# Optimization experiments

Measured on AMD Instinct MI355X. Metric: run time of the kernel, lower is better.

The kernel has to match this reference:

```python
import jax, jax.numpy as jnp
import numpy as np

NUM_HEADS = 10
DICT = 20  # attention_dictionary_size
BATCH = 262144


def setup_inputs() -> dict:
    key = jax.random.key(0)
    ks = jax.random.split(key, 6)
    x = jax.random.normal(ks[0], (BATCH, DICT), dtype=jnp.float32)
    # torch nn.Linear(20, 200, bias=False) weights: shape [out, in] = [200, 20]
    W1 = jax.random.normal(ks[1], (NUM_HEADS * DICT, DICT), dtype=jnp.float32) * 0.1
    W2 = jax.random.normal(ks[2], (NUM_HEADS * DICT, DICT), dtype=jnp.float32) * 0.1
    W3 = jax.random.normal(ks[3], (NUM_HEADS * DICT, DICT), dtype=jnp.float32) * 0.1
    W4 = jax.random.normal(ks[4], (NUM_HEADS * DICT, DICT), dtype=jnp.float32) * 0.1
    gamma = jax.random.normal(ks[5], (1,), dtype=jnp.float32)
    return {"x": x, "W1": W1, "W2": W2, "W3": W3, "W4": W4, "gamma": gamma}


def reference(x, W1, W2, W3, W4, gamma):
    B = x.shape[0]
    m = 1
    inp = x[:, None, :]                                   # [B, 1, 20]
    # Four bias-free projections: y = x @ W.T -> [B, 1, 200]
    q = (inp @ W1.T).reshape(NUM_HEADS, B, m, DICT)       # faithful .view (mixes batch/head)
    k = (inp @ W2.T).reshape(NUM_HEADS, B, DICT, m)
    v = (inp @ W3.T).reshape(NUM_HEADS, B, m, DICT)
    inner = q @ k                                         # [10, B, 1, 1]
    att = jax.nn.softmax(inner, axis=-1)                  # length-1 softmax -> ones (faithful)
    res = jnp.swapaxes(att, -1, -2) @ v                   # [10, B, 1, 20]
    res = res.reshape(B, m, NUM_HEADS * DICT)             # [B, 1, 200]
    out = jax.nn.relu(gamma * res + inp @ W4.T)           # [B, 1, 200]
    return out
```

## Files before the change

### kernel.cpp

```cpp
#include <hip/hip_runtime.h>


#define BATCH          262144
#define DICT           20
#define COLS           200
#define NTHREADS       256
#define ROWS_PER_BLOCK 128
#define NBLOCKS        (BATCH / ROWS_PER_BLOCK)

__global__ __launch_bounds__(NTHREADS)
void attn_collapsed_kernel(const float* __restrict__ x,
                           const float* __restrict__ W3,
                           const float* __restrict__ W4,
                           const float* __restrict__ gamma,
                           float* __restrict__ out)
{
    __shared__ float4 ldsM[COLS * 5];

    const int t = threadIdx.x;
    const float g = gamma[0];

    const float4* w3 = (const float4*)W3;
    const float4* w4 = (const float4*)W4;
    for (int i = t; i < COLS * 5; i += NTHREADS) {
        float4 a = w3[i], b = w4[i], m;
        m.x = fmaf(g, a.x, b.x);
        m.y = fmaf(g, a.y, b.y);
        m.z = fmaf(g, a.z, b.z);
        m.w = fmaf(g, a.w, b.w);
        ldsM[i] = m;
    }
    __syncthreads();

    const int row     = blockIdx.x * ROWS_PER_BLOCK + (t & 127);
    const int colbase = (t >> 7) * 100;

    float4 xv[5];
    {
        const float4* xr = (const float4*)(x + row * DICT);
#pragma unroll
        for (int i = 0; i < 5; ++i) xv[i] = xr[i];
    }

    float4* op = (float4*)(out + row * COLS + colbase);

#pragma unroll 5
    for (int c = 0; c < 25; ++c) {
        const float4* wp = &ldsM[(colbase + 4 * c) * 5];
        float4 acc;
        float* accp = (float*)&acc;
#pragma unroll
        for (int cc = 0; cc < 4; ++cc) {
            float p0 = 0.f, p1 = 0.f;
#pragma unroll
            for (int kk = 0; kk < 5; ++kk) {
                float4 w = wp[cc * 5 + kk];
                p0 = fmaf(w.x, xv[kk].x, p0);
                p1 = fmaf(w.y, xv[kk].y, p1);
                p0 = fmaf(w.z, xv[kk].z, p0);
                p1 = fmaf(w.w, xv[kk].w, p1);
            }
            accp[cc] = fmaxf(p0 + p1, 0.f);
        }
        op[c] = acc;
    }
}

extern "C" void kernel_launch(void* const* d_in, const int* in_sizes, int n_in,
                              void* d_out, int out_size, void* d_ws, size_t ws_size,
                              hipStream_t stream) {
    const float* x     = (const float*)d_in[0];
    const float* W3    = (const float*)d_in[3];
    const float* W4    = (const float*)d_in[4];
    const float* gamma = (const float*)d_in[5];
    float* out = (float*)d_out;

    attn_collapsed_kernel<<<NBLOCKS, NTHREADS, 0, stream>>>(x, W3, W4, gamma, out);
}
```

Baseline: 290.0 us.

## Remap threads to output columns for coalesced stores and register-resident weights

Reassigns work so each thread owns one float4 of output columns and walks 32 rows, instead of one row per thread with strided column writes. Consecutive threads now write consecutive float4s of a row, so stores are coalesced. Each thread keeps its 80 weight values in registers rather than reading LDS per row, and x rows are prefetched one iteration ahead. In exchange, 56 of the 256 threads per block sit idle, x loads become broadcast reads of the same row across threads, and register pressure rises.

```diff
diff --git a/kernel.cpp b/kernel.cpp
--- a/kernel.cpp
+++ b/kernel.cpp
@@ -5,11 +5,14 @@
 #define DICT           20
 #define COLS           200
 #define NTHREADS       256
+#define NGROUPS        4
+#define ACTIVE         (50 * NGROUPS)
 #define ROWS_PER_BLOCK 128
+#define ROWS_PER_GROUP (ROWS_PER_BLOCK / NGROUPS)
 #define NBLOCKS        (BATCH / ROWS_PER_BLOCK)
 
 __global__ __launch_bounds__(NTHREADS)
-void attn_collapsed_kernel(const float* __restrict__ x,
+void attn_coalesced_kernel(const float* __restrict__ x,
                            const float* __restrict__ W3,
                            const float* __restrict__ W4,
                            const float* __restrict__ gamma,
@@ -32,37 +35,56 @@
     }
     __syncthreads();
 
-    const int row     = blockIdx.x * ROWS_PER_BLOCK + (t & 127);
-    const int colbase = (t >> 7) * 100;
+    if (t >= ACTIVE) return;
+
+    const int cf4 = t % 50;
+    const int grp = t / 50;
+
+    float4 m[4][5];
+    {
+        const float4* mp = &ldsM[cf4 * 20];
+#pragma unroll
+        for (int c = 0; c < 4; ++c)
+#pragma unroll
+            for (int k = 0; k < 5; ++k)
+                m[c][k] = mp[c * 5 + k];
+    }
+
+    const int row0 = blockIdx.x * ROWS_PER_BLOCK + grp * ROWS_PER_GROUP;
+    const float4* xr = (const float4*)(x + (size_t)row0 * DICT);
+    float4* op = (float4*)(out + (size_t)row0 * COLS) + cf4;
 
     float4 xv[5];
-    {
-        const float4* xr = (const float4*)(x + row * DICT);
 #pragma unroll
-        for (int i = 0; i < 5; ++i) xv[i] = xr[i];
-    }
+    for (int k = 0; k < 5; ++k) xv[k] = xr[k];
 
-    float4* op = (float4*)(out + row * COLS + colbase);
+    for (int r = 0; r < ROWS_PER_GROUP; ++r) {
+        float4 xn[5];
+        if (r + 1 < ROWS_PER_GROUP) {
+            const float4* xq = xr + (r + 1) * 5;
+#pragma unroll
+            for (int k = 0; k < 5; ++k) xn[k] = xq[k];
+        }
 
-#pragma unroll 5
-    for (int c = 0; c < 25; ++c) {
-        const float4* wp = &ldsM[(colbase + 4 * c) * 5];
         float4 acc;
-        float* accp = (float*)&acc;
+        float* ap = (float*)&acc;
 #pragma unroll
-        for (int cc = 0; cc < 4; ++cc) {
+        for (int c = 0; c < 4; ++c) {
             float p0 = 0.f, p1 = 0.f;
 #pragma unroll
-            for (int kk = 0; kk < 5; ++kk) {
-                float4 w = wp[cc * 5 + kk];
-                p0 = fmaf(w.x, xv[kk].x, p0);
-                p1 = fmaf(w.y, xv[kk].y, p1);
-                p0 = fmaf(w.z, xv[kk].z, p0);
-                p1 = fmaf(w.w, xv[kk].w, p1);
+            for (int k = 0; k < 5; ++k) {
+                p0 = fmaf(m[c][k].x, xv[k].x, p0);
+                p1 = fmaf(m[c][k].y, xv[k].y, p1);
+                p0 = fmaf(m[c][k].z, xv[k].z, p0);
+                p1 = fmaf(m[c][k].w, xv[k].w, p1);
             }
-            accp[cc] = fmaxf(p0 + p1, 0.f);
+            ap[c] = fmaxf(p0 + p1, 0.f);
         }
-        op[c] = acc;
+
+        op[r * 50] = acc;
+
+#pragma unroll
+        for (int k = 0; k < 5; ++k) xv[k] = xn[k];
     }
 }
 
@@ -75,5 +97,5 @@
     const float* gamma = (const float*)d_in[5];
     float* out = (float*)d_out;
 
-    attn_collapsed_kernel<<<NBLOCKS, NTHREADS, 0, stream>>>(x, W3, W4, gamma, out);
+    attn_coalesced_kernel<<<NBLOCKS, NTHREADS, 0, stream>>>(x, W3, W4, gamma, out);
 }
```

Result: slower. 334.8 us (+15.4%).

## Keep weights in registers, stage x in LDS, write contiguous columns per row

Applied to the files above, without the earlier changes.

The kernel now gives each thread two fixed output columns. Their fused gamma*W3+W4 weights are held in registers, and the block's x rows are staged in LDS. Before, each thread owned a row and wrote 100 strided columns. Now a wavefront writes contiguous float2 spans across one row, which coalesces the dominant output stores and removes the per-row weight reads from LDS. In exchange, 56 of 256 threads exit idle, each thread recomputes its weights from global memory, and the launch bounds hint changes.

```diff
diff --git a/kernel.cpp b/kernel.cpp
--- a/kernel.cpp
+++ b/kernel.cpp
@@ -5,64 +5,81 @@
 #define DICT           20
 #define COLS           200
 #define NTHREADS       256
+#define CPT            100
+#define NGROUPS        2
+#define ACTIVE         (CPT * NGROUPS)
 #define ROWS_PER_BLOCK 128
+#define ROWS_PER_GROUP (ROWS_PER_BLOCK / NGROUPS)
 #define NBLOCKS        (BATCH / ROWS_PER_BLOCK)
 
-__global__ __launch_bounds__(NTHREADS)
-void attn_collapsed_kernel(const float* __restrict__ x,
-                           const float* __restrict__ W3,
-                           const float* __restrict__ W4,
-                           const float* __restrict__ gamma,
-                           float* __restrict__ out)
+__global__ __launch_bounds__(NTHREADS, 4)
+void attn_v5_kernel(const float* __restrict__ x,
+                    const float* __restrict__ W3,
+                    const float* __restrict__ W4,
+                    const float* __restrict__ gamma,
+                    float* __restrict__ out)
 {
-    __shared__ float4 ldsM[COLS * 5];
+    __shared__ float4 ldsX[ROWS_PER_BLOCK * 5];
 
     const int t = threadIdx.x;
-    const float g = gamma[0];
 
-    const float4* w3 = (const float4*)W3;
-    const float4* w4 = (const float4*)W4;
-    for (int i = t; i < COLS * 5; i += NTHREADS) {
-        float4 a = w3[i], b = w4[i], m;
-        m.x = fmaf(g, a.x, b.x);
-        m.y = fmaf(g, a.y, b.y);
-        m.z = fmaf(g, a.z, b.z);
-        m.w = fmaf(g, a.w, b.w);
-        ldsM[i] = m;
-    }
+    const float4* xg = (const float4*)(x + (size_t)blockIdx.x * ROWS_PER_BLOCK * DICT);
+    for (int i = t; i < ROWS_PER_BLOCK * 5; i += NTHREADS)
+        ldsX[i] = xg[i];
     __syncthreads();
 
-    const int row     = blockIdx.x * ROWS_PER_BLOCK + (t & 127);
-    const int colbase = (t >> 7) * 100;
+    if (t >= ACTIVE) return;
 
-    float4 xv[5];
+    const float g   = gamma[0];
+    const int   c2  = t % CPT;
+    const int   grp = t / CPT;
+
+    float4 m0[5], m1[5];
     {
-        const float4* xr = (const float4*)(x + row * DICT);
+        const float4* a0 = (const float4*)(W3 + (2 * c2 + 0) * DICT);
+        const float4* b0 = (const float4*)(W4 + (2 * c2 + 0) * DICT);
+        const float4* a1 = (const float4*)(W3 + (2 * c2 + 1) * DICT);
+        const float4* b1 = (const float4*)(W4 + (2 * c2 + 1) * DICT);
 #pragma unroll
-        for (int i = 0; i < 5; ++i) xv[i] = xr[i];
+        for (int k = 0; k < 5; ++k) {
+            float4 p = a0[k], q = b0[k], r;
+            r.x = fmaf(g, p.x, q.x); r.y = fmaf(g, p.y, q.y);
+            r.z = fmaf(g, p.z, q.z); r.w = fmaf(g, p.w, q.w);
+            m0[k] = r;
+            float4 s = a1[k], u = b1[k], v;
+            v.x = fmaf(g, s.x, u.x); v.y = fmaf(g, s.y, u.y);
+            v.z = fmaf(g, s.z, u.z); v.w = fmaf(g, s.w, u.w);
+            m1[k] = v;
+        }
     }
 
-    float4* op = (float4*)(out + row * COLS + colbase);
+    const int row0 = blockIdx.x * ROWS_PER_BLOCK + grp * ROWS_PER_GROUP;
+    const float4* xl = &ldsX[grp * ROWS_PER_GROUP * 5];
+    float* ob = out + (size_t)row0 * COLS + 2 * c2;
 
-#pragma unroll 5
-    for (int c = 0; c < 25; ++c) {
-        const float4* wp = &ldsM[(colbase + 4 * c) * 5];
-        float4 acc;
-        float* accp = (float*)&acc;
+#pragma unroll 2
+    for (int r = 0; r < ROWS_PER_GROUP; ++r) {
+        float4 xv[5];
 #pragma unroll
-        for (int cc = 0; cc < 4; ++cc) {
-            float p0 = 0.f, p1 = 0.f;
+        for (int k = 0; k < 5; ++k) xv[k] = xl[r * 5 + k];
+
+        float p0 = 0.f, p1 = 0.f, q0 = 0.f, q1 = 0.f;
 #pragma unroll
-            for (int kk = 0; kk < 5; ++kk) {
-                float4 w = wp[cc * 5 + kk];
-                p0 = fmaf(w.x, xv[kk].x, p0);
-                p1 = fmaf(w.y, xv[kk].y, p1);
-                p0 = fmaf(w.z, xv[kk].z, p0);
-                p1 = fmaf(w.w, xv[kk].w, p1);
-            }
-            accp[cc] = fmaxf(p0 + p1, 0.f);
+        for (int k = 0; k < 5; ++k) {
+            p0 = fmaf(m0[k].x, xv[k].x, p0);
+            p1 = fmaf(m0[k].y, xv[k].y, p1);
+            p0 = fmaf(m0[k].z, xv[k].z, p0);
+            p1 = fmaf(m0[k].w, xv[k].w, p1);
+            q0 = fmaf(m1[k].x, xv[k].x, q0);
+            q1 = fmaf(m1[k].y, xv[k].y, q1);
+            q0 = fmaf(m1[k].z, xv[k].z, q0);
+            q1 = fmaf(m1[k].w, xv[k].w, q1);
         }
-        op[c] = acc;
+        float2 o;
+        o.x = fmaxf(p0 + p1, 0.f);
+        o.y = fmaxf(q0 + q1, 0.f);
+
+        *(float2*)(ob + (size_t)r * COLS) = o;
     }
 }
 
@@ -75,5 +92,5 @@
     const float* gamma = (const float*)d_in[5];
     float* out = (float*)d_out;
 
-    attn_collapsed_kernel<<<NBLOCKS, NTHREADS, 0, stream>>>(x, W3, W4, gamma, out);
+    attn_v5_kernel<<<NBLOCKS, NTHREADS, 0, stream>>>(x, W3, W4, gamma, out);
 }
```

New measurement: 253.5 us. -12.6%, faster.

## Keep combined weights in registers and write output rows coalesced per wave

Applied to the files above, without the earlier changes.

Each lane now holds four columns of the fused gamma*W3+W4 matrix in registers, and each wave walks 32 rows staged in LDS. A wave's store instruction writes one contiguous 800-byte output row, where before each thread wrote 100 strided floats. Loads and stores are marked nontemporal, and the next row's x is loaded while the current row is computed. This costs heavy register use and leaves 14 of 64 lanes idle.

```diff
diff --git a/kernel.cpp b/kernel.cpp
--- a/kernel.cpp
+++ b/kernel.cpp
@@ -6,64 +6,91 @@
 #define COLS           200
 #define NTHREADS       256
 #define ROWS_PER_BLOCK 128
+#define ROWS_PER_WAVE  32
 #define NBLOCKS        (BATCH / ROWS_PER_BLOCK)
 
-__global__ __launch_bounds__(NTHREADS)
-void attn_collapsed_kernel(const float* __restrict__ x,
-                           const float* __restrict__ W3,
-                           const float* __restrict__ W4,
-                           const float* __restrict__ gamma,
-                           float* __restrict__ out)
+typedef float f32x4 __attribute__((ext_vector_type(4)));
+
+__global__ __launch_bounds__(NTHREADS, 3)
+void attn_v6_kernel(const float* __restrict__ x,
+                    const float* __restrict__ W3,
+                    const float* __restrict__ W4,
+                    const float* __restrict__ gamma,
+                    float* __restrict__ out)
 {
-    __shared__ float4 ldsM[COLS * 5];
+    __shared__ f32x4 ldsX[ROWS_PER_BLOCK * 5];
 
     const int t = threadIdx.x;
-    const float g = gamma[0];
 
-    const float4* w3 = (const float4*)W3;
-    const float4* w4 = (const float4*)W4;
-    for (int i = t; i < COLS * 5; i += NTHREADS) {
-        float4 a = w3[i], b = w4[i], m;
-        m.x = fmaf(g, a.x, b.x);
-        m.y = fmaf(g, a.y, b.y);
-        m.z = fmaf(g, a.z, b.z);
-        m.w = fmaf(g, a.w, b.w);
-        ldsM[i] = m;
-    }
+    const f32x4* xg = (const f32x4*)(x + (size_t)blockIdx.x * ROWS_PER_BLOCK * DICT);
+    for (int i = t; i < ROWS_PER_BLOCK * 5; i += NTHREADS)
+        ldsX[i] = __builtin_nontemporal_load(&xg[i]);
     __syncthreads();
 
-    const int row     = blockIdx.x * ROWS_PER_BLOCK + (t & 127);
-    const int colbase = (t >> 7) * 100;
+    const int lane = t & 63;
+    const int wv   = t >> 6;
+    if (lane >= 50) return;
 
-    float4 xv[5];
-    {
-        const float4* xr = (const float4*)(x + row * DICT);
+    const float g   = gamma[0];
+    const int   cf4 = lane;
+
+    f32x4 m[4][5];
 #pragma unroll
-        for (int i = 0; i < 5; ++i) xv[i] = xr[i];
+    for (int c = 0; c < 4; ++c) {
+        const f32x4* a = (const f32x4*)(W3 + (4 * cf4 + c) * DICT);
+        const f32x4* b = (const f32x4*)(W4 + (4 * cf4 + c) * DICT);
+#pragma unroll
+        for (int k = 0; k < 5; ++k) {
+            f32x4 p = a[k], q = b[k], r;
+            r.x = fmaf(g, p.x, q.x); r.y = fmaf(g, p.y, q.y);
+            r.z = fmaf(g, p.z, q.z); r.w = fmaf(g, p.w, q.w);
+            m[c][k] = r;
+        }
     }
 
-    float4* op = (float4*)(out + row * COLS + colbase);
+    const int row0 = blockIdx.x * ROWS_PER_BLOCK + wv * ROWS_PER_WAVE;
+    const f32x4* xl = &ldsX[wv * ROWS_PER_WAVE * 5];
+    f32x4* op = (f32x4*)(out + (size_t)row0 * COLS) + cf4;
 
-#pragma unroll 5
-    for (int c = 0; c < 25; ++c) {
-        const float4* wp = &ldsM[(colbase + 4 * c) * 5];
-        float4 acc;
-        float* accp = (float*)&acc;
+#define DOT4(ACC, XV)                                          \
+    {                                                          \
+        float* ap_ = (float*)&(ACC);                           \
+        _Pragma("unroll")                                      \
+        for (int c = 0; c < 4; ++c) {                          \
+            float p0 = 0.f, p1 = 0.f;                          \
+            _Pragma("unroll")                                  \
+            for (int k = 0; k < 5; ++k) {                      \
+                p0 = fmaf(m[c][k].x, (XV)[k].x, p0);           \
+                p1 = fmaf(m[c][k].y, (XV)[k].y, p1);           \
+                p0 = fmaf(m[c][k].z, (XV)[k].z, p0);           \
+                p1 = fmaf(m[c][k].w, (XV)[k].w, p1);           \
+            }                                                  \
+            ap_[c] = fmaxf(p0 + p1, 0.f);                      \
+        }                                                      \
+    }
+
+    f32x4 xv[5], xn[5];
 #pragma unroll
-        for (int cc = 0; cc < 4; ++cc) {
-            float p0 = 0.f, p1 = 0.f;
+    for (int k = 0; k < 5; ++k) xv[k] = xl[k];
+
+    for (int r = 0; r < ROWS_PER_WAVE; r += 2) {
 #pragma unroll
-            for (int kk = 0; kk < 5; ++kk) {
-                float4 w = wp[cc * 5 + kk];
-                p0 = fmaf(w.x, xv[kk].x, p0);
-                p1 = fmaf(w.y, xv[kk].y, p1);
-                p0 = fmaf(w.z, xv[kk].z, p0);
-                p1 = fmaf(w.w, xv[kk].w, p1);
-            }
-            accp[cc] = fmaxf(p0 + p1, 0.f);
+        for (int k = 0; k < 5; ++k) xn[k] = xl[(r + 1) * 5 + k];
+
+        f32x4 acc0;
+        DOT4(acc0, xv)
+        __builtin_nontemporal_store(acc0, &op[(size_t)r * 50]);
+
+        if (r + 2 < ROWS_PER_WAVE) {
+#pragma unroll
+            for (int k = 0; k < 5; ++k) xv[k] = xl[(r + 2) * 5 + k];
         }
-        op[c] = acc;
+
+        f32x4 acc1;
+        DOT4(acc1, xn)
+        __builtin_nontemporal_store(acc1, &op[(size_t)(r + 1) * 50]);
     }
+#undef DOT4
 }
 
 extern "C" void kernel_launch(void* const* d_in, const int* in_sizes, int n_in,
@@ -75,5 +102,5 @@
     const float* gamma = (const float*)d_in[5];
     float* out = (float*)d_out;
 
-    attn_collapsed_kernel<<<NBLOCKS, NTHREADS, 0, stream>>>(x, W3, W4, gamma, out);
+    attn_v6_kernel<<<NBLOCKS, NTHREADS, 0, stream>>>(x, W3, W4, gamma, out);
 }
```

Result: faster. 248.3 us (-14.4%).
